# Kernel optimization log

Measured on AMD Instinct MI355X. Metric: run time of the kernel, lower is better.

The kernel has to match this reference:

```python
import jax, jax.numpy as jnp
import numpy as np

B = 16384          # batch_size
NF = 50            # n_fields
K = 16             # embedding_dim
V = 1_000_000      # input_dim (vocab)
H = 400            # fc hidden
NNZ = B * NF


def _xavier(key, shape):
    fan_in, fan_out = shape
    lim = (6.0 / (fan_in + fan_out)) ** 0.5
    return jax.random.uniform(key, shape, minval=-lim, maxval=lim, dtype=jnp.float32)


def setup_inputs() -> dict:
    key = jax.random.key(0)
    ks = jax.random.split(key, 12)
    feats = jax.random.randint(ks[0], (NNZ,), 0, V)
    # n_fields contiguous features per sample (required by view(batch_size,-1))
    index = jnp.repeat(jnp.arange(B), NF)
    values = jax.random.uniform(ks[1], (NNZ,), dtype=jnp.float32)
    bias = jnp.zeros((1, 1), jnp.float32)
    weights = _xavier(ks[2], (V, 1))
    embedding = _xavier(ks[3], (V, K))
    d = NF * K  # 800
    W0 = _xavier(ks[4], (d, H))
    b0 = jax.random.normal(ks[5], (1, 1), jnp.float32)
    W1 = _xavier(ks[6], (H, H))
    b1 = jax.random.normal(ks[7], (1, 1), jnp.float32)
    W2 = _xavier(ks[8], (H, 1))
    b2 = jax.random.normal(ks[9], (1, 1), jnp.float32)
    return dict(index=index, feats=feats, values=values, bias=bias,
                weights=weights, embedding=embedding,
                W0=W0, b0=b0, W1=W1, b1=b1, W2=W2, b2=b2, batch_size=B)


def reference(index, feats, values, bias, weights, embedding,
              W0, b0, W1, b1, W2, b2, batch_size):
    # gather (F.embedding)
    w = weights[feats, 0]              # [nnz]
    emb = embedding[feats]             # [nnz, K]

    # first order: segment-sum of w*v, plus bias ([B] + [1,1] -> [1,B], as in torch)
    first = jax.ops.segment_sum(w * values, index, num_segments=batch_size) + bias

    # second order: FM pooling trick, fused over all K dims in one segment reduce
    ev = emb * values[:, None]                                        # [nnz, K]
    s1 = jax.ops.segment_sum(ev, index, num_segments=batch_size)      # [B, K]
    s2 = jax.ops.segment_sum(ev * ev, index, num_segments=batch_size) # [B, K]
    second = 0.5 * jnp.sum(s1 * s1 - s2, axis=1)                      # [B]

    # higher order MLP (relu on every layer, scalar biases)
    x = emb.reshape(batch_size, -1)    # [B, NF*K]
    x = jax.nn.relu(x @ W0 + b0)
    x = jax.nn.relu(x @ W1 + b1)
    x = jax.nn.relu(x @ W2 + b2)       # [B, 1]
    higher = x.reshape(-1)             # [B]

    return jax.nn.sigmoid(first + second + higher)  # [1, B]
```

## Files before the change

kernel.cpp:

```cpp
#include <hip/hip_runtime.h>
#include <hip/hip_bf16.h>


#define BATCH 16384
#define NFLD  50
#define EK    16
#define DDIM  800
#define HDIM  400
#define HPAD  416
#define NPAD  512

#define TB_W0 400
#define TB_W1 208
#define TBLK  (TB_W0 + TB_W1)
#define GBLK  (BATCH / 16)

#define MROWS 64
#define NCOLS 448
#define WCOLS 112
#define NFRAG 7
#define P1    (DDIM / 32)
#define P2    (HPAD / 32)
#define H0S   424

#define PH1B(b) ((b) * 32768)
#define PH2B(b) ((b) * 28672)
#define H0OFF   98304
#define REDOFF  152576
#define LDSSZ   153600

#define VMCNT(N) asm volatile("s_waitcnt vmcnt(" #N ")" ::: "memory")

typedef __attribute__((ext_vector_type(8))) __bf16 bf16x8;
typedef __attribute__((ext_vector_type(4))) float  f32x4;

typedef const __attribute__((address_space(1))) unsigned int* gas_u32p;
typedef __attribute__((address_space(3))) unsigned int*       las_u32p;

__device__ __forceinline__ void gld_lds16(const void* g, void* l) {
    __builtin_amdgcn_global_load_lds((gas_u32p)g, (las_u32p)l, 16, 0, 0);
}

__device__ __forceinline__ void bar() {
    __builtin_amdgcn_sched_barrier(0);
    __builtin_amdgcn_s_barrier();
    __builtin_amdgcn_sched_barrier(0);
}

__global__ __launch_bounds__(256) void prep_kernel(
    const float* __restrict__ W0, const float* __restrict__ W1,
    __hip_bfloat16* __restrict__ W0t, __hip_bfloat16* __restrict__ W1t,
    const int* __restrict__ feats, const float* __restrict__ values,
    const float* __restrict__ biasp, const float* __restrict__ weights,
    const float* __restrict__ embedding,
    float* __restrict__ fs, __hip_bfloat16* __restrict__ x)
{
    const int bid = blockIdx.x;
    if (bid < TBLK) {
        const int which = bid >= TB_W0;
        const int i  = which ? bid - TB_W0 : bid;
        const int nx = which ? 13 : 25;
        const int bx = i % nx, by = i / nx;
        const float* src = which ? W1 : W0;
        __hip_bfloat16* dst = which ? W1t : W0t;
        const int srcK = which ? HDIM : DDIM;
        const int dstCols = which ? HPAD : DDIM;

        __shared__ float tile[32][33];
        const int tx = threadIdx.x & 31, ty = threadIdx.x >> 5;
        const int k0 = bx * 32, n0 = by * 32;
#pragma unroll
        for (int r = 0; r < 4; ++r) {
            int k = k0 + ty + r * 8;
            int n = n0 + tx;
            float v = (k < srcK && n < HDIM) ? src[(long)k * HDIM + n] : 0.f;
            tile[ty + r * 8][tx] = v;
        }
        __syncthreads();
#pragma unroll
        for (int r = 0; r < 4; ++r) {
            int n = n0 + ty + r * 8;
            int k = k0 + tx;
            if (k < dstCols)
                dst[(long)n * dstCols + k] = __float2bfloat16(tile[tx][ty + r * 8]);
        }
        return;
    }

    const int wave = threadIdx.x >> 6;
    const int lane = threadIdx.x & 63;
    const int r    = lane >> 2, c = lane & 3;
    const int sbase = (bid - TBLK) * 16 + wave * 4;

    int   f[4] = {0, 0, 0, 0};
    float v[4] = {0.f, 0.f, 0.f, 0.f};
    float wsum[4] = {0.f, 0.f, 0.f, 0.f};
#pragma unroll
    for (int q = 0; q < 4; ++q) {
        const long base = (long)(sbase + q) * NFLD;
        if (lane < NFLD) {
            f[q] = feats[base + lane];
            v[q] = values[base + lane];
            wsum[q] = weights[f[q]] * v[q];
        }
    }

    int   fj[4][4]; float vj[4][4];
#pragma unroll
    for (int q = 0; q < 4; ++q)
#pragma unroll
        for (int p = 0; p < 4; ++p) {
            const int j = p * 16 + r;
            if (p < 3 || r < 2) {
                fj[q][p] = __shfl(f[q], j);
                vj[q][p] = __shfl(v[q], j);
            }
        }
    float4 e[4][4];
#pragma unroll
    for (int q = 0; q < 4; ++q)
#pragma unroll
        for (int p = 0; p < 4; ++p)
            if (p < 3 || r < 2)
                e[q][p] = *(const float4*)(embedding + (long)fj[q][p] * EK + c * 4);

#pragma unroll
    for (int q = 0; q < 4; ++q) {
        const int s = sbase + q;
        f32x4 s1 = {0.f, 0.f, 0.f, 0.f}, s2 = {0.f, 0.f, 0.f, 0.f};
#pragma unroll
        for (int p = 0; p < 4; ++p) {
            const int j = p * 16 + r;
            if (p < 3 || r < 2) {
                f32x4 ef = {e[q][p].x, e[q][p].y, e[q][p].z, e[q][p].w};
                f32x4 ev = ef * vj[q][p];
                s1 += ev;
                s2 += ev * ev;
                __hip_bfloat16 pk[4] = {
                    __float2bfloat16(e[q][p].x), __float2bfloat16(e[q][p].y),
                    __float2bfloat16(e[q][p].z), __float2bfloat16(e[q][p].w)};
                *(uint2*)&x[(long)s * DDIM + j * EK + c * 4] = *(uint2*)pk;
            }
        }
#pragma unroll
        for (int m = 4; m <= 32; m <<= 1) {
            s1.x += __shfl_xor(s1.x, m); s1.y += __shfl_xor(s1.y, m);
            s1.z += __shfl_xor(s1.z, m); s1.w += __shfl_xor(s1.w, m);
            s2.x += __shfl_xor(s2.x, m); s2.y += __shfl_xor(s2.y, m);
            s2.z += __shfl_xor(s2.z, m); s2.w += __shfl_xor(s2.w, m);
        }
        float t = (s1.x * s1.x - s2.x) + (s1.y * s1.y - s2.y)
                + (s1.z * s1.z - s2.z) + (s1.w * s1.w - s2.w);
        t += __shfl_xor(t, 1); t += __shfl_xor(t, 2);
        float w = wsum[q];
        w += __shfl_xor(w, 1);  w += __shfl_xor(w, 2);
        w += __shfl_xor(w, 4);  w += __shfl_xor(w, 8);
        w += __shfl_xor(w, 16); w += __shfl_xor(w, 32);
        if (lane == 0) fs[s] = w + 0.5f * t + biasp[0];
    }
}

__global__ __launch_bounds__(512, 2) void fused_mlp_kernel(
    const __hip_bfloat16* __restrict__ x,
    const __hip_bfloat16* __restrict__ W0t, const __hip_bfloat16* __restrict__ W1t,
    const float* __restrict__ b0p, const float* __restrict__ b1p,
    const float* __restrict__ W2, const float* __restrict__ b2p,
    const float* __restrict__ fs, float* __restrict__ out)
{
    __shared__ __align__(16) char lds[LDSSZ];
    __hip_bfloat16* h0p = (__hip_bfloat16*)(lds + H0OFF);
    float*          red = (float*)(lds + REDOFF);

    const int tid  = threadIdx.x;
    const int wave = tid >> 6, lane = tid & 63;
    const int l16  = lane & 15, quad = lane >> 4;
    const int waveM = wave & 1, waveN = wave >> 1;
    const int m0 = blockIdx.x * MROWS;

    const int rl  = lane >> 2;
    const int swc = ((lane & 3) ^ ((lane >> 3) & 3)) * 8;
    const int qsw = (quad ^ ((l16 >> 1) & 3)) * 8;

    const float b0 = b0p[0];
    const float b1 = b1p[0];

    auto stage1 = [&](int p, int b) {
        const int k0 = p * 32;
        char* dst = lds + PH1B(b);
#pragma unroll
        for (int c = 0; c < 4; ++c) {
            const int idx = wave * 4 + c;
            const __hip_bfloat16* src = (idx < 4)
                ? x   + (long)(m0 + idx * 16 + rl) * DDIM + k0 + swc
                : W0t + (long)((idx - 4) * 16 + rl) * DDIM + k0 + swc;
            gld_lds16(src, dst + idx * 1024 + lane * 16);
        }
    };

    f32x4 acc[2][NFRAG] = {};
    auto compute1 = [&](int b) {
        const __hip_bfloat16* s = (const __hip_bfloat16*)(lds + PH1B(b));
        bf16x8 af[2], bfr[NFRAG];
#pragma unroll
        for (int i = 0; i < 2; ++i)
            af[i] = *(const bf16x8*)&s[(waveM * 2 + i) * 512 + l16 * 32 + qsw];
#pragma unroll
        for (int j = 0; j < NFRAG; ++j)
            bfr[j] = *(const bf16x8*)&s[(4 + waveN * NFRAG + j) * 512 + l16 * 32 + qsw];
        __builtin_amdgcn_s_setprio(1);
#pragma unroll
        for (int i = 0; i < 2; ++i)
#pragma unroll
            for (int j = 0; j < NFRAG; ++j)
                acc[i][j] = __builtin_amdgcn_mfma_f32_16x16x32_bf16(
                    af[i], bfr[j], acc[i][j], 0, 0, 0);
        __builtin_amdgcn_s_setprio(0);
    };

    stage1(0, 0);
    stage1(1, 1);
    for (int p = 0; p < P1; ++p) {
        if (p + 1 < P1) { VMCNT(4); } else { VMCNT(0); }
        bar();
        if (p + 2 < P1) stage1(p + 2, (p + 2) % 3);
        compute1(p % 3);
    }
    bar();

    auto stage2 = [&](int p, int b) {
        if (wave < 7) {
            const int k0 = p * 32;
#pragma unroll
            for (int c = 0; c < 4; ++c) {
                const int ch = wave * 4 + c;
                gld_lds16(W1t + (long)(ch * 16 + rl) * HPAD + k0 + swc,
                          lds + PH2B(b) + ch * 1024 + lane * 16);
            }
        }
    };
    stage2(0, 0);
    stage2(1, 1);

#pragma unroll
    for (int i = 0; i < 2; ++i)
#pragma unroll
        for (int j = 0; j < NFRAG; ++j) {
            const int col = waveN * WCOLS + j * 16 + l16;
            if (col < HPAD) {
#pragma unroll
                for (int r = 0; r < 4; ++r) {
                    const int row = waveM * 32 + i * 16 + quad * 4 + r;
                    float v = acc[i][j][r] + b0;
                    v = v > 0.f ? v : 0.f;
                    if (col >= HDIM) v = 0.f;
                    h0p[row * H0S + col] = __float2bfloat16(v);
                }
            }
        }

    f32x4 acc2[2][NFRAG] = {};
    float w2v[NFRAG];
#pragma unroll
    for (int j = 0; j < NFRAG; ++j) {
        const int col = waveN * WCOLS + j * 16 + l16;
        w2v[j] = (col < HDIM) ? W2[col] : 0.f;
    }
    auto compute2 = [&](int p, int b) {
        const __hip_bfloat16* s = (const __hip_bfloat16*)(lds + PH2B(b));
        bf16x8 af[2], bfr[NFRAG];
#pragma unroll
        for (int i = 0; i < 2; ++i)
            af[i] = *(const bf16x8*)&h0p[(waveM * 32 + i * 16 + l16) * H0S + p * 32 + quad * 8];
#pragma unroll
        for (int j = 0; j < NFRAG; ++j)
            bfr[j] = *(const bf16x8*)&s[(waveN * NFRAG + j) * 512 + l16 * 32 + qsw];
        __builtin_amdgcn_s_setprio(1);
#pragma unroll
        for (int i = 0; i < 2; ++i)
#pragma unroll
            for (int j = 0; j < NFRAG; ++j)
                acc2[i][j] = __builtin_amdgcn_mfma_f32_16x16x32_bf16(
                    af[i], bfr[j], acc2[i][j], 0, 0, 0);
        __builtin_amdgcn_s_setprio(0);
    };

    asm volatile("s_waitcnt lgkmcnt(0)" ::: "memory");
    bar();

    for (int p = 0; p < P2; ++p) {
        if (p + 1 < P2) { VMCNT(4); } else { VMCNT(0); }
        bar();
        if (p + 2 < P2) stage2(p + 2, (p + 2) % 3);
        compute2(p, p % 3);
    }

#pragma unroll
    for (int i = 0; i < 2; ++i)
#pragma unroll
        for (int r = 0; r < 4; ++r) {
            float ps = 0.f;
#pragma unroll
            for (int j = 0; j < NFRAG; ++j) {
                float v = acc2[i][j][r] + b1;
                v = v > 0.f ? v : 0.f;
                ps += v * w2v[j];
            }
            ps += __shfl_xor(ps, 1); ps += __shfl_xor(ps, 2);
            ps += __shfl_xor(ps, 4); ps += __shfl_xor(ps, 8);
            if (l16 == 0)
                red[(waveM * 32 + i * 16 + quad * 4 + r) * 4 + waveN] = ps;
        }
    __syncthreads();

    if (tid < MROWS) {
        const float4 rr = *(const float4*)&red[tid * 4];
        const float s = (rr.x + rr.y) + (rr.z + rr.w);
        float hv = s + b2p[0];
        hv = hv > 0.f ? hv : 0.f;
        const float z = fs[m0 + tid] + hv;
        out[m0 + tid] = 1.f / (1.f + __expf(-z));
    }
}

extern "C" void kernel_launch(void* const* d_in, const int* in_sizes, int n_in,
                              void* d_out, int out_size, void* d_ws, size_t ws_size,
                              hipStream_t stream)
{
    const int*   feats     = (const int*)d_in[1];
    const float* values    = (const float*)d_in[2];
    const float* bias      = (const float*)d_in[3];
    const float* weights   = (const float*)d_in[4];
    const float* embedding = (const float*)d_in[5];
    const float* W0 = (const float*)d_in[6];
    const float* b0 = (const float*)d_in[7];
    const float* W1 = (const float*)d_in[8];
    const float* b1 = (const float*)d_in[9];
    const float* W2 = (const float*)d_in[10];
    const float* b2 = (const float*)d_in[11];

    char* ws = (char*)d_ws;
    size_t off = 0;
    auto alloc = [&](size_t bytes) {
        void* p = ws + off;
        off += (bytes + 255) & ~(size_t)255;
        return p;
    };
    float*          fs   = (float*)alloc((size_t)BATCH * 4);
    __hip_bfloat16* x    = (__hip_bfloat16*)alloc((size_t)BATCH * DDIM * 2);
    __hip_bfloat16* W0t  = (__hip_bfloat16*)alloc((size_t)NPAD * DDIM * 2);
    __hip_bfloat16* W1t  = (__hip_bfloat16*)alloc((size_t)NPAD * HPAD * 2);
    (void)ws_size; (void)in_sizes; (void)n_in; (void)out_size;

    prep_kernel<<<dim3(TBLK + GBLK), 256, 0, stream>>>(
        W0, W1, W0t, W1t, feats, values, bias, weights, embedding, fs, x);
    fused_mlp_kernel<<<dim3(BATCH / MROWS), 512, 0, stream>>>(
        x, W0t, W1t, b0, b1, W2, b2, fs, (float*)d_out);
}
```

Before: 165.9 us.

## Keep full activation tile in LDS and stream weight fragments from global to registers

Rewrites the fused MLP kernel so the 64x800 activation tile is loaded into LDS once, and each of 8 waves computes 64 output columns. The weight B-fragments for both layers are loaded directly from global memory into double-buffered registers. This removes per-k-step barriers and the LDS staging of weights, and lowers LDS use enough to possibly allow more blocks per CU. In exchange, global load latency is exposed in the MFMA loop, and padding to 512 columns adds wasted MFMA work and may read past the padded weight rows.

```diff
diff --git a/kernel.cpp b/kernel.cpp
--- a/kernel.cpp
+++ b/kernel.cpp
@@ -16,18 +16,12 @@
 #define GBLK  (BATCH / 16)
 
 #define MROWS 64
-#define NCOLS 448
-#define WCOLS 112
-#define NFRAG 7
 #define P1    (DDIM / 32)
 #define P2    (HPAD / 32)
 #define H0S   424
 
-#define PH1B(b) ((b) * 32768)
-#define PH2B(b) ((b) * 28672)
-#define H0OFF   98304
-#define REDOFF  152576
-#define LDSSZ   153600
+#define REDOFF  102400
+#define LDSSZ   104448
 
 #define VMCNT(N) asm volatile("s_waitcnt vmcnt(" #N ")" ::: "memory")
 
@@ -168,14 +162,15 @@
     const float* __restrict__ fs, float* __restrict__ out)
 {
     __shared__ __align__(16) char lds[LDSSZ];
-    __hip_bfloat16* h0p = (__hip_bfloat16*)(lds + H0OFF);
-    float*          red = (float*)(lds + REDOFF);
+    __hip_bfloat16* apan = (__hip_bfloat16*)lds;
+    __hip_bfloat16* h0p  = (__hip_bfloat16*)lds;
+    float*          red  = (float*)(lds + REDOFF);
 
     const int tid  = threadIdx.x;
     const int wave = tid >> 6, lane = tid & 63;
     const int l16  = lane & 15, quad = lane >> 4;
-    const int waveM = wave & 1, waveN = wave >> 1;
     const int m0 = blockIdx.x * MROWS;
+    const int nbase = wave * 64;
 
     const int rl  = lane >> 2;
     const int swc = ((lane & 3) ^ ((lane >> 3) & 3)) * 8;
@@ -184,72 +179,73 @@
     const float b0 = b0p[0];
     const float b1 = b1p[0];
 
-    auto stage1 = [&](int p, int b) {
-        const int k0 = p * 32;
-        char* dst = lds + PH1B(b);
-#pragma unroll
-        for (int c = 0; c < 4; ++c) {
-            const int idx = wave * 4 + c;
-            const __hip_bfloat16* src = (idx < 4)
-                ? x   + (long)(m0 + idx * 16 + rl) * DDIM + k0 + swc
-                : W0t + (long)((idx - 4) * 16 + rl) * DDIM + k0 + swc;
-            gld_lds16(src, dst + idx * 1024 + lane * 16);
-        }
-    };
-
-    f32x4 acc[2][NFRAG] = {};
-    auto compute1 = [&](int b) {
-        const __hip_bfloat16* s = (const __hip_bfloat16*)(lds + PH1B(b));
-        bf16x8 af[2], bfr[NFRAG];
-#pragma unroll
-        for (int i = 0; i < 2; ++i)
-            af[i] = *(const bf16x8*)&s[(waveM * 2 + i) * 512 + l16 * 32 + qsw];
-#pragma unroll
-        for (int j = 0; j < NFRAG; ++j)
-            bfr[j] = *(const bf16x8*)&s[(4 + waveN * NFRAG + j) * 512 + l16 * 32 + qsw];
+#pragma unroll
+    for (int c = 0; c < 13; ++c) {
+        const int id = c * 8 + wave;
+        if (id < 100)
+            gld_lds16(x + (long)(m0 + (id & 3) * 16 + rl) * DDIM + (id >> 2) * 32 + swc,
+                      lds + id * 1024 + lane * 16);
+    }
+    VMCNT(0);
+    bar();
+
+    f32x4 acc[4][4] = {};
+    const __hip_bfloat16* bp1 = W0t + (long)(nbase + l16) * DDIM + quad * 8;
+
+    auto loadB1 = [&](int p, bf16x8* bb) {
+#pragma unroll
+        for (int j = 0; j < 4; ++j)
+            bb[j] = *(const bf16x8*)(bp1 + (long)j * 16 * DDIM + p * 32);
+    };
+    auto comp1 = [&](int p, const bf16x8* bb) {
+        bf16x8 af[4];
+#pragma unroll
+        for (int i = 0; i < 4; ++i)
+            af[i] = *(const bf16x8*)&apan[p * 2048 + i * 512 + l16 * 32 + qsw];
         __builtin_amdgcn_s_setprio(1);
 #pragma unroll
-        for (int i = 0; i < 2; ++i)
-#pragma unroll
-            for (int j = 0; j < NFRAG; ++j)
+        for (int i = 0; i < 4; ++i)
+#pragma unroll
+            for (int j = 0; j < 4; ++j)
                 acc[i][j] = __builtin_amdgcn_mfma_f32_16x16x32_bf16(
-                    af[i], bfr[j], acc[i][j], 0, 0, 0);
+                    af[i], bb[j], acc[i][j], 0, 0, 0);
         __builtin_amdgcn_s_setprio(0);
     };
 
-    stage1(0, 0);
-    stage1(1, 1);
-    for (int p = 0; p < P1; ++p) {
-        if (p + 1 < P1) { VMCNT(4); } else { VMCNT(0); }
-        bar();
-        if (p + 2 < P1) stage1(p + 2, (p + 2) % 3);
-        compute1(p % 3);
-    }
+    {
+        bf16x8 bA[4], bB[4];
+        loadB1(0, bA);
+        loadB1(1, bB);
+        for (int p = 0; p < P1 - 1; p += 2) {
+            comp1(p, bA);
+            if (p + 2 < P1) loadB1(p + 2, bA);
+            comp1(p + 1, bB);
+            if (p + 3 < P1) loadB1(p + 3, bB);
+        }
+        comp1(P1 - 1, bA);
+    }
+
+    const __hip_bfloat16* bp2 = W1t + (long)(nbase + l16) * HPAD + quad * 8;
+    auto loadB2 = [&](int p, bf16x8* bb) {
+#pragma unroll
+        for (int j = 0; j < 4; ++j)
+            bb[j] = *(const bf16x8*)(bp2 + (long)j * 16 * HPAD + p * 32);
+    };
+    bf16x8 cA[4], cB[4];
+    loadB2(0, cA);
+    loadB2(1, cB);
+
     bar();
 
-    auto stage2 = [&](int p, int b) {
-        if (wave < 7) {
-            const int k0 = p * 32;
-#pragma unroll
-            for (int c = 0; c < 4; ++c) {
-                const int ch = wave * 4 + c;
-                gld_lds16(W1t + (long)(ch * 16 + rl) * HPAD + k0 + swc,
-                          lds + PH2B(b) + ch * 1024 + lane * 16);
-            }
-        }
-    };
-    stage2(0, 0);
-    stage2(1, 1);
-
-#pragma unroll
-    for (int i = 0; i < 2; ++i)
-#pragma unroll
-        for (int j = 0; j < NFRAG; ++j) {
-            const int col = waveN * WCOLS + j * 16 + l16;
+#pragma unroll
+    for (int i = 0; i < 4; ++i)
+#pragma unroll
+        for (int j = 0; j < 4; ++j) {
+            const int col = nbase + j * 16 + l16;
             if (col < HPAD) {
 #pragma unroll
                 for (int r = 0; r < 4; ++r) {
-                    const int row = waveM * 32 + i * 16 + quad * 4 + r;
+                    const int row = i * 16 + quad * 4 + r;
                     float v = acc[i][j][r] + b0;
                     v = v > 0.f ? v : 0.f;
                     if (col >= HDIM) v = 0.f;
@@ -257,50 +253,46 @@
                 }
             }
         }
-
-    f32x4 acc2[2][NFRAG] = {};
-    float w2v[NFRAG];
-#pragma unroll
-    for (int j = 0; j < NFRAG; ++j) {
-        const int col = waveN * WCOLS + j * 16 + l16;
-        w2v[j] = (col < HDIM) ? W2[col] : 0.f;
-    }
-    auto compute2 = [&](int p, int b) {
-        const __hip_bfloat16* s = (const __hip_bfloat16*)(lds + PH2B(b));
-        bf16x8 af[2], bfr[NFRAG];
-#pragma unroll
-        for (int i = 0; i < 2; ++i)
-            af[i] = *(const bf16x8*)&h0p[(waveM * 32 + i * 16 + l16) * H0S + p * 32 + quad * 8];
-#pragma unroll
-        for (int j = 0; j < NFRAG; ++j)
-            bfr[j] = *(const bf16x8*)&s[(waveN * NFRAG + j) * 512 + l16 * 32 + qsw];
-        __builtin_amdgcn_s_setprio(1);
-#pragma unroll
-        for (int i = 0; i < 2; ++i)
-#pragma unroll
-            for (int j = 0; j < NFRAG; ++j)
-                acc2[i][j] = __builtin_amdgcn_mfma_f32_16x16x32_bf16(
-                    af[i], bfr[j], acc2[i][j], 0, 0, 0);
-        __builtin_amdgcn_s_setprio(0);
-    };
-
     asm volatile("s_waitcnt lgkmcnt(0)" ::: "memory");
     bar();
 
-    for (int p = 0; p < P2; ++p) {
-        if (p + 1 < P2) { VMCNT(4); } else { VMCNT(0); }
-        bar();
-        if (p + 2 < P2) stage2(p + 2, (p + 2) % 3);
-        compute2(p, p % 3);
-    }
-
-#pragma unroll
-    for (int i = 0; i < 2; ++i)
+    f32x4 acc2[4][4] = {};
+    auto comp2 = [&](int p, const bf16x8* bb) {
+        bf16x8 af[4];
+#pragma unroll
+        for (int i = 0; i < 4; ++i)
+            af[i] = *(const bf16x8*)&h0p[(i * 16 + l16) * H0S + p * 32 + quad * 8];
+        __builtin_amdgcn_s_setprio(1);
+#pragma unroll
+        for (int i = 0; i < 4; ++i)
+#pragma unroll
+            for (int j = 0; j < 4; ++j)
+                acc2[i][j] = __builtin_amdgcn_mfma_f32_16x16x32_bf16(
+                    af[i], bb[j], acc2[i][j], 0, 0, 0);
+        __builtin_amdgcn_s_setprio(0);
+    };
+
+    for (int p = 0; p < P2 - 1; p += 2) {
+        comp2(p, cA);
+        if (p + 2 < P2) loadB2(p + 2, cA);
+        comp2(p + 1, cB);
+        if (p + 3 < P2) loadB2(p + 3, cB);
+    }
+    comp2(P2 - 1, cA);
+
+    float w2v[4];
+#pragma unroll
+    for (int j = 0; j < 4; ++j) {
+        const int col = nbase + j * 16 + l16;
+        w2v[j] = (col < HDIM) ? W2[col] : 0.f;
+    }
+#pragma unroll
+    for (int i = 0; i < 4; ++i)
 #pragma unroll
         for (int r = 0; r < 4; ++r) {
             float ps = 0.f;
 #pragma unroll
-            for (int j = 0; j < NFRAG; ++j) {
+            for (int j = 0; j < 4; ++j) {
                 float v = acc2[i][j][r] + b1;
                 v = v > 0.f ? v : 0.f;
                 ps += v * w2v[j];
@@ -308,13 +300,15 @@
             ps += __shfl_xor(ps, 1); ps += __shfl_xor(ps, 2);
             ps += __shfl_xor(ps, 4); ps += __shfl_xor(ps, 8);
             if (l16 == 0)
-                red[(waveM * 32 + i * 16 + quad * 4 + r) * 4 + waveN] = ps;
+                red[(i * 16 + quad * 4 + r) * 8 + wave] = ps;
         }
     __syncthreads();
 
     if (tid < MROWS) {
-        const float4 rr = *(const float4*)&red[tid * 4];
-        const float s = (rr.x + rr.y) + (rr.z + rr.w);
+        const float4 r0 = *(const float4*)&red[tid * 8];
+        const float4 r1 = *(const float4*)&red[tid * 8 + 4];
+        const float s = ((r0.x + r0.y) + (r0.z + r0.w))
+                      + ((r1.x + r1.y) + (r1.z + r1.w));
         float hv = s + b2p[0];
         hv = hv > 0.f ? hv : 0.f;
         const float z = fs[m0 + tid] + hv;
```

Measured after the change: 171.2 us. 3.2% more time.

## Retile fused MLP to 7 waves each owning 64 columns across all 64 rows

Applied to the files above, without the earlier changes.

Changes the fused MLP kernel from 8 waves in a 2x4 grid (32 rows x 112 columns each) to 7 waves that each compute all 64 rows by 64 columns with a 4x4 MFMA fragment grid. Block size drops to 448 threads. Global-to-LDS staging is redistributed as 5 or 4 chunks per wave, and the final reduction buffer is widened to 8 slots per row. The aim is to cut wasted padded-column MFMAs, since 448 columns previously needed 7 fragments per wave. It also balances A/B fragment reuse per wave. In exchange there are fewer waves per block, more accumulator registers per wave, and the occupancy hint of 2 blocks is dropped.

```diff
diff --git a/kernel.cpp b/kernel.cpp
--- a/kernel.cpp
+++ b/kernel.cpp
@@ -17,8 +17,6 @@
 
 #define MROWS 64
 #define NCOLS 448
-#define WCOLS 112
-#define NFRAG 7
 #define P1    (DDIM / 32)
 #define P2    (HPAD / 32)
 #define H0S   424
@@ -27,7 +25,7 @@
 #define PH2B(b) ((b) * 28672)
 #define H0OFF   98304
 #define REDOFF  152576
-#define LDSSZ   153600
+#define LDSSZ   154624
 
 #define VMCNT(N) asm volatile("s_waitcnt vmcnt(" #N ")" ::: "memory")
 
@@ -160,7 +158,7 @@
     }
 }
 
-__global__ __launch_bounds__(512, 2) void fused_mlp_kernel(
+__global__ __launch_bounds__(448) void fused_mlp_kernel(
     const __hip_bfloat16* __restrict__ x,
     const __hip_bfloat16* __restrict__ W0t, const __hip_bfloat16* __restrict__ W1t,
     const float* __restrict__ b0p, const float* __restrict__ b1p,
@@ -174,8 +172,8 @@
     const int tid  = threadIdx.x;
     const int wave = tid >> 6, lane = tid & 63;
     const int l16  = lane & 15, quad = lane >> 4;
-    const int waveM = wave & 1, waveN = wave >> 1;
     const int m0 = blockIdx.x * MROWS;
+    const int nbase = wave * 64;
 
     const int rl  = lane >> 2;
     const int swc = ((lane & 3) ^ ((lane >> 3) & 3)) * 8;
@@ -184,34 +182,38 @@
     const float b0 = b0p[0];
     const float b1 = b1p[0];
 
+    const int sstart = (wave < 4) ? wave * 5 : 20 + (wave - 4) * 4;
+    const int scnt   = (wave < 4) ? 5 : 4;
     auto stage1 = [&](int p, int b) {
         const int k0 = p * 32;
         char* dst = lds + PH1B(b);
 #pragma unroll
-        for (int c = 0; c < 4; ++c) {
-            const int idx = wave * 4 + c;
-            const __hip_bfloat16* src = (idx < 4)
-                ? x   + (long)(m0 + idx * 16 + rl) * DDIM + k0 + swc
-                : W0t + (long)((idx - 4) * 16 + rl) * DDIM + k0 + swc;
-            gld_lds16(src, dst + idx * 1024 + lane * 16);
-        }
-    };
-
-    f32x4 acc[2][NFRAG] = {};
+        for (int c = 0; c < 5; ++c) {
+            if (c < scnt) {
+                const int id = sstart + c;
+                const __hip_bfloat16* src = (id < 4)
+                    ? x   + (long)(m0 + id * 16 + rl) * DDIM + k0 + swc
+                    : W0t + (long)((id - 4) * 16 + rl) * DDIM + k0 + swc;
+                gld_lds16(src, dst + id * 1024 + lane * 16);
+            }
+        }
+    };
+
+    f32x4 acc[4][4] = {};
     auto compute1 = [&](int b) {
         const __hip_bfloat16* s = (const __hip_bfloat16*)(lds + PH1B(b));
-        bf16x8 af[2], bfr[NFRAG];
-#pragma unroll
-        for (int i = 0; i < 2; ++i)
-            af[i] = *(const bf16x8*)&s[(waveM * 2 + i) * 512 + l16 * 32 + qsw];
-#pragma unroll
-        for (int j = 0; j < NFRAG; ++j)
-            bfr[j] = *(const bf16x8*)&s[(4 + waveN * NFRAG + j) * 512 + l16 * 32 + qsw];
+        bf16x8 af[4], bfr[4];
+#pragma unroll
+        for (int i = 0; i < 4; ++i)
+            af[i] = *(const bf16x8*)&s[i * 512 + l16 * 32 + qsw];
+#pragma unroll
+        for (int j = 0; j < 4; ++j)
+            bfr[j] = *(const bf16x8*)&s[(4 + wave * 4 + j) * 512 + l16 * 32 + qsw];
         __builtin_amdgcn_s_setprio(1);
 #pragma unroll
-        for (int i = 0; i < 2; ++i)
-#pragma unroll
-            for (int j = 0; j < NFRAG; ++j)
+        for (int i = 0; i < 4; ++i)
+#pragma unroll
+            for (int j = 0; j < 4; ++j)
                 acc[i][j] = __builtin_amdgcn_mfma_f32_16x16x32_bf16(
                     af[i], bfr[j], acc[i][j], 0, 0, 0);
         __builtin_amdgcn_s_setprio(0);
@@ -228,28 +230,26 @@
     bar();
 
     auto stage2 = [&](int p, int b) {
-        if (wave < 7) {
-            const int k0 = p * 32;
-#pragma unroll
-            for (int c = 0; c < 4; ++c) {
-                const int ch = wave * 4 + c;
-                gld_lds16(W1t + (long)(ch * 16 + rl) * HPAD + k0 + swc,
-                          lds + PH2B(b) + ch * 1024 + lane * 16);
-            }
+        const int k0 = p * 32;
+#pragma unroll
+        for (int c = 0; c < 4; ++c) {
+            const int ch = wave * 4 + c;
+            gld_lds16(W1t + (long)(ch * 16 + rl) * HPAD + k0 + swc,
+                      lds + PH2B(b) + ch * 1024 + lane * 16);
         }
     };
     stage2(0, 0);
     stage2(1, 1);
 
 #pragma unroll
-    for (int i = 0; i < 2; ++i)
-#pragma unroll
-        for (int j = 0; j < NFRAG; ++j) {
-            const int col = waveN * WCOLS + j * 16 + l16;
+    for (int i = 0; i < 4; ++i)
+#pragma unroll
+        for (int j = 0; j < 4; ++j) {
+            const int col = nbase + j * 16 + l16;
             if (col < HPAD) {
 #pragma unroll
                 for (int r = 0; r < 4; ++r) {
-                    const int row = waveM * 32 + i * 16 + quad * 4 + r;
+                    const int row = i * 16 + quad * 4 + r;
                     float v = acc[i][j][r] + b0;
                     v = v > 0.f ? v : 0.f;
                     if (col >= HDIM) v = 0.f;
@@ -258,27 +258,27 @@
             }
         }
 
-    f32x4 acc2[2][NFRAG] = {};
-    float w2v[NFRAG];
-#pragma unroll
-    for (int j = 0; j < NFRAG; ++j) {
-        const int col = waveN * WCOLS + j * 16 + l16;
+    f32x4 acc2[4][4] = {};
+    float w2v[4];
+#pragma unroll
+    for (int j = 0; j < 4; ++j) {
+        const int col = nbase + j * 16 + l16;
         w2v[j] = (col < HDIM) ? W2[col] : 0.f;
     }
     auto compute2 = [&](int p, int b) {
         const __hip_bfloat16* s = (const __hip_bfloat16*)(lds + PH2B(b));
-        bf16x8 af[2], bfr[NFRAG];
-#pragma unroll
-        for (int i = 0; i < 2; ++i)
-            af[i] = *(const bf16x8*)&h0p[(waveM * 32 + i * 16 + l16) * H0S + p * 32 + quad * 8];
-#pragma unroll
-        for (int j = 0; j < NFRAG; ++j)
-            bfr[j] = *(const bf16x8*)&s[(waveN * NFRAG + j) * 512 + l16 * 32 + qsw];
+        bf16x8 af[4], bfr[4];
+#pragma unroll
+        for (int i = 0; i < 4; ++i)
+            af[i] = *(const bf16x8*)&h0p[(i * 16 + l16) * H0S + p * 32 + quad * 8];
+#pragma unroll
+        for (int j = 0; j < 4; ++j)
+            bfr[j] = *(const bf16x8*)&s[(wave * 4 + j) * 512 + l16 * 32 + qsw];
         __builtin_amdgcn_s_setprio(1);
 #pragma unroll
-        for (int i = 0; i < 2; ++i)
-#pragma unroll
-            for (int j = 0; j < NFRAG; ++j)
+        for (int i = 0; i < 4; ++i)
+#pragma unroll
+            for (int j = 0; j < 4; ++j)
                 acc2[i][j] = __builtin_amdgcn_mfma_f32_16x16x32_bf16(
                     af[i], bfr[j], acc2[i][j], 0, 0, 0);
         __builtin_amdgcn_s_setprio(0);
@@ -294,13 +294,14 @@
         compute2(p, p % 3);
     }
 
-#pragma unroll
-    for (int i = 0; i < 2; ++i)
+    if (tid < MROWS) red[tid * 8 + 7] = 0.f;
+#pragma unroll
+    for (int i = 0; i < 4; ++i)
 #pragma unroll
         for (int r = 0; r < 4; ++r) {
             float ps = 0.f;
 #pragma unroll
-            for (int j = 0; j < NFRAG; ++j) {
+            for (int j = 0; j < 4; ++j) {
                 float v = acc2[i][j][r] + b1;
                 v = v > 0.f ? v : 0.f;
                 ps += v * w2v[j];
@@ -308,13 +309,15 @@
             ps += __shfl_xor(ps, 1); ps += __shfl_xor(ps, 2);
             ps += __shfl_xor(ps, 4); ps += __shfl_xor(ps, 8);
             if (l16 == 0)
-                red[(waveM * 32 + i * 16 + quad * 4 + r) * 4 + waveN] = ps;
+                red[(i * 16 + quad * 4 + r) * 8 + wave] = ps;
         }
     __syncthreads();
 
     if (tid < MROWS) {
-        const float4 rr = *(const float4*)&red[tid * 4];
-        const float s = (rr.x + rr.y) + (rr.z + rr.w);
+        const float4 r0 = *(const float4*)&red[tid * 8];
+        const float4 r1 = *(const float4*)&red[tid * 8 + 4];
+        const float s = ((r0.x + r0.y) + (r0.z + r0.w))
+                      + ((r1.x + r1.y) + (r1.z + r1.w));
         float hv = s + b2p[0];
         hv = hv > 0.f ? hv : 0.f;
         const float z = fs[m0 + tid] + hv;
@@ -353,6 +356,6 @@
 
     prep_kernel<<<dim3(TBLK + GBLK), 256, 0, stream>>>(
         W0, W1, W0t, W1t, feats, values, bias, weights, embedding, fs, x);
-    fused_mlp_kernel<<<dim3(BATCH / MROWS), 512, 0, stream>>>(
+    fused_mlp_kernel<<<dim3(BATCH / MROWS), 448, 0, stream>>>(
         x, W0t, W1t, b0, b1, W2, b2, fs, (float*)d_out);
 }
```

New measurement: 167.5 us. About the same (+0.9%).
